# Kernel optimization log

Measured on AMD Instinct MI355X. Metric: run time of the kernel, lower is better.

The kernel has to match this reference:

```python
import jax, jax.numpy as jnp
import numpy as np

DIM = 512
NUM_HEADS = 8
HEAD_SIZE = 64
INNER = NUM_HEADS * HEAD_SIZE  # 512


def setup_inputs() -> dict:
    key = jax.random.key(0)
    k1, k2, k3, k4, k5 = jax.random.split(key, 5)
    x = jax.random.normal(k1, (2, 4096, DIM), dtype=jnp.float32)
    # Linear params stored as [in, out] for y = x @ W + b (same math as torch Linear)
    w_qkv = jax.random.normal(k2, (DIM, INNER * 3), dtype=jnp.float32) * (1.0 / np.sqrt(DIM))
    b_qkv = jax.random.normal(k3, (INNER * 3,), dtype=jnp.float32) * 0.01
    w_out = jax.random.normal(k4, (INNER, DIM), dtype=jnp.float32) * (1.0 / np.sqrt(INNER))
    b_out = jax.random.normal(k5, (DIM,), dtype=jnp.float32) * 0.01
    return {"x": x, "w_qkv": w_qkv, "b_qkv": b_qkv, "w_out": w_out, "b_out": b_out}


def reference(x, w_qkv, b_qkv, w_out, b_out):
    b, n, _ = x.shape
    qkv = x @ w_qkv + b_qkv                      # [b, n, 3*inner]
    q, k, v = jnp.split(qkv, 3, axis=-1)          # each [b, n, inner]

    def heads(t):  # 'b n (h d) -> b h n d'
        return t.reshape(b, n, NUM_HEADS, HEAD_SIZE).transpose(0, 2, 1, 3)

    q, k, v = heads(q), heads(k), heads(v)
    scores = jnp.einsum('bhnd,bhmd->bhnm', q, k) / jnp.sqrt(jnp.float32(HEAD_SIZE))
    probs = jax.nn.softmax(scores, axis=-1)       # dropout is identity in eval
    out = jnp.einsum('bhnm,bhmd->bhnd', probs, v)
    out = out.transpose(0, 2, 1, 3).reshape(b, n, INNER)  # 'b h n d -> b n (h d)'
    return out @ w_out + b_out
```

## Files before the change

kernel.cpp:

```cpp
#include <hip/hip_runtime.h>

typedef __bf16 bf16;
typedef __bf16 bf16x8 __attribute__((ext_vector_type(8)));
typedef float f32x4 __attribute__((ext_vector_type(4)));
typedef unsigned u32x4 __attribute__((ext_vector_type(4)));

#define MFMA16(a, b, c) __builtin_amdgcn_mfma_f32_16x16x32_bf16((a), (b), (c), 0, 0, 0)

static __device__ __forceinline__ bf16x8 ldg8(const bf16* p) {
  return *(const bf16x8*)p;
}
static __device__ __forceinline__ unsigned cvt_pk_bf16(float lo, float hi) {
  unsigned d;
  asm("v_cvt_pk_bf16_f32 %0, %1, %2" : "=v"(d) : "v"(lo), "v"(hi));
  return d;
}
static __device__ __forceinline__ void pl32_swap(unsigned& a, unsigned& b) {
  asm("v_permlane32_swap_b32 %0, %1" : "+v"(a), "+v"(b));
}
static __device__ __forceinline__ void pl16_swap(unsigned& a, unsigned& b) {
  asm("v_permlane16_swap_b32 %0, %1" : "+v"(a), "+v"(b));
}


__global__ __launch_bounds__(256) void cvt_pack_x(const float* __restrict__ x,
                                                  bf16* __restrict__ Xp) {
  int mt = blockIdx.x, kc = blockIdx.y;
  int r = threadIdx.x >> 1;
  int khalf = threadIdx.x & 1;
  const float* src = x + (size_t)(mt * 128 + r) * 512 + kc * 32 + khalf * 16;
  float4 v0 = *(const float4*)(src + 0);
  float4 v1 = *(const float4*)(src + 4);
  float4 v2 = *(const float4*)(src + 8);
  float4 v3 = *(const float4*)(src + 12);
  bf16* tile = Xp + ((size_t)mt * 16 + kc) * 4096;
  bf16x8 a, b;
  a[0] = (bf16)v0.x; a[1] = (bf16)v0.y; a[2] = (bf16)v0.z; a[3] = (bf16)v0.w;
  a[4] = (bf16)v1.x; a[5] = (bf16)v1.y; a[6] = (bf16)v1.z; a[7] = (bf16)v1.w;
  b[0] = (bf16)v2.x; b[1] = (bf16)v2.y; b[2] = (bf16)v2.z; b[3] = (bf16)v2.w;
  b[4] = (bf16)v3.x; b[5] = (bf16)v3.y; b[6] = (bf16)v3.z; b[7] = (bf16)v3.w;
  int kc0 = khalf * 2;
  *(bf16x8*)&tile[(kc0 + 0) * 1024 + r * 8] = a;
  *(bf16x8*)&tile[(kc0 + 1) * 1024 + r * 8] = b;
}

__global__ __launch_bounds__(256) void transpose_pack_w(const float* __restrict__ W,
                                                        bf16* __restrict__ Wp,
                                                        int N) {
  __shared__ float tile[32 * 129];
  int kc = blockIdx.x, nt = blockIdx.y;
  int row = threadIdx.x >> 3;
  int c0 = (threadIdx.x & 7) * 16;
  const float* src = W + (size_t)(kc * 32 + row) * N + nt * 128 + c0;
#pragma unroll
  for (int i = 0; i < 4; i++) {
    float4 v = *(const float4*)(src + i * 4);
    tile[row * 129 + c0 + i * 4 + 0] = v.x;
    tile[row * 129 + c0 + i * 4 + 1] = v.y;
    tile[row * 129 + c0 + i * 4 + 2] = v.z;
    tile[row * 129 + c0 + i * 4 + 3] = v.w;
  }
  __syncthreads();
  bf16* dst = Wp + ((size_t)nt * 16 + kc) * 4096;
#pragma unroll
  for (int half = 0; half < 2; half++) {
    int U = threadIdx.x + half * 256;
    int kchunk = U >> 7, n = U & 127;
    bf16x8 o;
#pragma unroll
    for (int j = 0; j < 8; j++) o[j] = (bf16)tile[(kchunk * 8 + j) * 129 + n];
    *(bf16x8*)&dst[U * 8] = o;
  }
}

__device__ __forceinline__ void gemm128_core(const bf16* __restrict__ At,
                                             const bf16* __restrict__ Bt,
                                             bf16* Ab0, bf16* Ab1, bf16* Bb0,
                                             bf16* Bb1, int tid, int wr, int wc,
                                             int l16, int quad, f32x4 acc[4][4]) {
  bf16x8 pa0 = ldg8(At + tid * 8);
  bf16x8 pa1 = ldg8(At + 2048 + tid * 8);
  bf16x8 pb0 = ldg8(Bt + tid * 8);
  bf16x8 pb1 = ldg8(Bt + 2048 + tid * 8);
#pragma unroll 2
  for (int kc = 0; kc < 16; kc++) {
    bf16* Ab = (kc & 1) ? Ab1 : Ab0;
    bf16* Bb = (kc & 1) ? Bb1 : Bb0;
    *(bf16x8*)&Ab[tid * 8] = pa0;
    *(bf16x8*)&Ab[2048 + tid * 8] = pa1;
    *(bf16x8*)&Bb[tid * 8] = pb0;
    *(bf16x8*)&Bb[2048 + tid * 8] = pb1;
    __syncthreads();
    if (kc < 15) {
      const bf16* an = At + (kc + 1) * 4096;
      const bf16* bn = Bt + (kc + 1) * 4096;
      pa0 = ldg8(an + tid * 8);
      pa1 = ldg8(an + 2048 + tid * 8);
      pb0 = ldg8(bn + tid * 8);
      pb1 = ldg8(bn + 2048 + tid * 8);
    }
    bf16x8 af[4], bf[4];
#pragma unroll
    for (int fi = 0; fi < 4; fi++)
      af[fi] = *(const bf16x8*)&Ab[(quad * 128 + wr * 64 + fi * 16 + l16) * 8];
#pragma unroll
    for (int fj = 0; fj < 4; fj++)
      bf[fj] = *(const bf16x8*)&Bb[(quad * 128 + wc * 64 + fj * 16 + l16) * 8];
    __builtin_amdgcn_s_setprio(1);
#pragma unroll
    for (int fi = 0; fi < 4; fi++)
#pragma unroll
      for (int fj = 0; fj < 4; fj++)
        acc[fi][fj] = MFMA16(af[fi], bf[fj], acc[fi][fj]);
    __builtin_amdgcn_s_setprio(0);
  }
}

__global__ __launch_bounds__(256, 3) void qkv_gemm(const bf16* __restrict__ Xp,
                                                   const bf16* __restrict__ Wp1,
                                                   const float* __restrict__ bqkv,
                                                   bf16* __restrict__ Q,
                                                   bf16* __restrict__ Kh,
                                                   bf16* __restrict__ Vt) {
  int mt = blockIdx.x, nt = blockIdx.y;
  int tid = threadIdx.x;
  int wave = tid >> 6, lane = tid & 63;
  int l16 = lane & 15, quad = lane >> 4;
  int wr = wave >> 1, wc = wave & 1;

  __shared__ __align__(16) bf16 Ab[2][4096];
  __shared__ __align__(16) bf16 Bb[2][4096];

  f32x4 acc[4][4] = {};
  gemm128_core(Xp + (size_t)mt * 16 * 4096, Wp1 + (size_t)nt * 16 * 4096,
               Ab[0], Ab[1], Bb[0], Bb[1], tid, wr, wc, l16, quad, acc);

#pragma unroll
  for (int fj = 0; fj < 4; fj++) {
    int c = nt * 128 + wc * 64 + fj * 16 + l16;
    float bias = bqkv[c];
    int which = c >> 9, inner = c & 511;
    int h = inner >> 6, d = inner & 63;
#pragma unroll
    for (int fi = 0; fi < 4; fi++) {
#pragma unroll
      for (int r = 0; r < 4; r++) {
        int m = mt * 128 + wr * 64 + fi * 16 + quad * 4 + r;
        int b = m >> 12, n = m & 4095;
        int bh = b * 8 + h;
        float v = acc[fi][fj][r] + bias;
        if (which == 0)
          Q[((size_t)bh * 4096 + n) * 64 + d] = (bf16)(v * 0.18033688f);
        else if (which == 1)
          Kh[((size_t)bh * 4096 + n) * 64 + d] = (bf16)v;
        else
          Vt[(((size_t)bh * 64 + (n >> 6)) * 64 + d) * 64 + (n & 63)] = (bf16)v;
      }
    }
  }
}

__global__ __launch_bounds__(256, 4) void flash_partial(const bf16* __restrict__ Q,
                                                        const bf16* __restrict__ K,
                                                        const bf16* __restrict__ Vt,
                                                        bf16* __restrict__ Opart,
                                                        float* __restrict__ Lpart) {
  int strip = blockIdx.x, bh = blockIdx.y, half = blockIdx.z;
  int tid = threadIdx.x;
  int wave = tid >> 6, lane = tid & 63;
  int l16 = lane & 15, quad = lane >> 4;

  const bf16* Qh = Q + (size_t)bh * 4096 * 64;
  const bf16* Kg = K + ((size_t)bh * 4096 + half * 2048) * 64;
  const bf16* Vg = Vt + (size_t)bh * 64 * 4096 + (size_t)half * 2048 * 64;

  __shared__ __align__(16) bf16 Klds[2][4096];
  __shared__ __align__(16) bf16 Vlds[2][4096];

  int qbase = strip * 128 + wave * 32;
  bf16x8 aq[2][2];
#pragma unroll
  for (int mt = 0; mt < 2; mt++) {
    const bf16* qr = Qh + (size_t)(qbase + mt * 16 + l16) * 64;
    aq[mt][0] = ldg8(qr + quad * 8);
    aq[mt][1] = ldg8(qr + 32 + quad * 8);
  }

  bf16x8 ones;
#pragma unroll
  for (int i = 0; i < 8; i++) ones[i] = (bf16)1.0f;

  f32x4 o[2][4] = {};
  f32x4 acc_l[2] = {};

  int e0 = tid * 8, e1 = (256 + tid) * 8;
  int r0 = e0 >> 6, r1 = e1 >> 6;
  int u0 = r0 * 8 + (((e0 & 63) >> 3) ^ (r0 & 7));
  int u1 = r1 * 8 + (((e1 & 63) >> 3) ^ (r1 & 7));

  bf16x8 kp0 = ldg8(Kg + e0), kp1 = ldg8(Kg + e1);
  bf16x8 vp0 = ldg8(Vg + e0), vp1 = ldg8(Vg + e1);

#pragma unroll 2
  for (int t = 0; t < 32; t++) {
    int cur = t & 1;
    bf16* kl = Klds[cur];
    bf16* vl = Vlds[cur];
    *(bf16x8*)&kl[u0 * 8] = kp0;
    *(bf16x8*)&kl[u1 * 8] = kp1;
    *(bf16x8*)&vl[u0 * 8] = vp0;
    *(bf16x8*)&vl[u1 * 8] = vp1;
    __syncthreads();

    if (t < 31) {
      const bf16* kg = Kg + (size_t)(t + 1) * 4096;
      const bf16* vg = Vg + (size_t)(t + 1) * 4096;
      kp0 = ldg8(kg + e0);
      kp1 = ldg8(kg + e1);
      vp0 = ldg8(vg + e0);
      vp1 = ldg8(vg + e1);
    }

    f32x4 s[2][2][2] = {};
    __builtin_amdgcn_s_setprio(1);
#pragma unroll
    for (int h2 = 0; h2 < 2; h2++)
#pragma unroll
      for (int c2 = 0; c2 < 2; c2++) {
        int n = h2 * 32 + c2 * 16 + l16;
        bf16x8 k0 = *(const bf16x8*)&kl[(n * 8 + (quad ^ (n & 7))) * 8];
        bf16x8 k1 = *(const bf16x8*)&kl[(n * 8 + ((4 + quad) ^ (n & 7))) * 8];
#pragma unroll
        for (int mt = 0; mt < 2; mt++) {
          s[h2][mt][c2] = MFMA16(k0, aq[mt][0], s[h2][mt][c2]);
          s[h2][mt][c2] = MFMA16(k1, aq[mt][1], s[h2][mt][c2]);
        }
      }
    __builtin_amdgcn_s_setprio(0);

    bf16x8 pa[2][2];
#pragma unroll
    for (int h2 = 0; h2 < 2; h2++)
#pragma unroll
      for (int mt = 0; mt < 2; mt++) {
        unsigned ue[2], wo[2];
#pragma unroll
        for (int c2 = 0; c2 < 2; c2++) {
          float p0 = __builtin_amdgcn_exp2f(s[h2][mt][c2][0]);
          float p1 = __builtin_amdgcn_exp2f(s[h2][mt][c2][1]);
          float p2 = __builtin_amdgcn_exp2f(s[h2][mt][c2][2]);
          float p3 = __builtin_amdgcn_exp2f(s[h2][mt][c2][3]);
          ue[c2] = cvt_pk_bf16(p0, p1);
          wo[c2] = cvt_pk_bf16(p2, p3);
        }
        pl32_swap(ue[0], ue[1]);
        pl16_swap(ue[0], ue[1]);
        pl32_swap(wo[0], wo[1]);
        pl16_swap(wo[0], wo[1]);
        u32x4 pk = {ue[0], wo[0], ue[1], wo[1]};
        pa[h2][mt] = __builtin_bit_cast(bf16x8, pk);
      }

    __builtin_amdgcn_s_setprio(1);
    acc_l[0] = MFMA16(pa[0][0], ones, acc_l[0]);
    acc_l[1] = MFMA16(pa[0][1], ones, acc_l[1]);
    acc_l[0] = MFMA16(pa[1][0], ones, acc_l[0]);
    acc_l[1] = MFMA16(pa[1][1], ones, acc_l[1]);
#pragma unroll
    for (int h2 = 0; h2 < 2; h2++)
#pragma unroll
      for (int ct = 0; ct < 4; ct++) {
        int d = ct * 16 + l16;
        bf16x8 bv = *(const bf16x8*)&vl[(d * 8 + ((h2 * 4 + quad) ^ (d & 7))) * 8];
        o[0][ct] = MFMA16(pa[h2][0], bv, o[0][ct]);
        o[1][ct] = MFMA16(pa[h2][1], bv, o[1][ct]);
      }
    __builtin_amdgcn_s_setprio(0);
  }

  size_t ub = ((size_t)half * 16 + bh) * 32 + strip;
  bf16* op = Opart + ub * 8192;
#pragma unroll
  for (int mt = 0; mt < 2; mt++) {
#pragma unroll
    for (int ct = 0; ct < 4; ct++)
#pragma unroll
      for (int r = 0; r < 4; r++)
        op[(wave * 32 + mt * 16 + quad * 4 + r) * 64 + ct * 16 + l16] =
            (bf16)o[mt][ct][r];
    if (l16 == 0) {
#pragma unroll
      for (int r = 0; r < 4; r++)
        Lpart[ub * 128 + wave * 32 + mt * 16 + quad * 4 + r] = acc_l[mt][r];
    }
  }
}

__global__ __launch_bounds__(256) void flash_combine(const bf16* __restrict__ Opart,
                                                     const float* __restrict__ Lpart,
                                                     bf16* __restrict__ Ap) {
  int mt = blockIdx.x, kc = blockIdx.y;
  int b = mt >> 5, strip = mt & 31;
  int h = kc >> 1, d0 = (kc & 1) * 32;
  int bh = b * 8 + h;
  size_t u0 = (size_t)bh * 32 + strip;
  size_t u1 = ((size_t)16 + bh) * 32 + strip;
  bf16* dst = Ap + ((size_t)mt * 16 + kc) * 4096;
#pragma unroll
  for (int hf = 0; hf < 2; hf++) {
    int U = threadIdx.x + hf * 256;
    int kchunk = U >> 7, r = U & 127;
    bf16x8 o0 = ldg8(&Opart[u0 * 8192 + r * 64 + d0 + kchunk * 8]);
    bf16x8 o1 = ldg8(&Opart[u1 * 8192 + r * 64 + d0 + kchunk * 8]);
    float ls = Lpart[u0 * 128 + r] + Lpart[u1 * 128 + r];
    float rl = 1.0f / ls;
    bf16x8 ov;
#pragma unroll
    for (int j = 0; j < 8; j++) ov[j] = (bf16)(((float)o0[j] + (float)o1[j]) * rl);
    *(bf16x8*)&dst[U * 8] = ov;
  }
}

__global__ __launch_bounds__(256, 3) void out_gemm(const bf16* __restrict__ Ap,
                                                   const bf16* __restrict__ Wp2,
                                                   const float* __restrict__ bout,
                                                   float* __restrict__ Out) {
  int mt = blockIdx.x, nt = blockIdx.y;
  int tid = threadIdx.x;
  int wave = tid >> 6, lane = tid & 63;
  int l16 = lane & 15, quad = lane >> 4;
  int wr = wave >> 1, wc = wave & 1;

  __shared__ __align__(16) bf16 Ab[2][4096];
  __shared__ __align__(16) bf16 Bb[2][4096];

  f32x4 acc[4][4] = {};
  gemm128_core(Ap + (size_t)mt * 16 * 4096, Wp2 + (size_t)nt * 16 * 4096,
               Ab[0], Ab[1], Bb[0], Bb[1], tid, wr, wc, l16, quad, acc);

#pragma unroll
  for (int fj = 0; fj < 4; fj++) {
    int c = nt * 128 + wc * 64 + fj * 16 + l16;
    float bias = bout[c];
#pragma unroll
    for (int fi = 0; fi < 4; fi++) {
#pragma unroll
      for (int r = 0; r < 4; r++) {
        int m = mt * 128 + wr * 64 + fi * 16 + quad * 4 + r;
        Out[(size_t)m * 512 + c] = acc[fi][fj][r] + bias;
      }
    }
  }
}

extern "C" void kernel_launch(void* const* d_in, const int* in_sizes, int n_in,
                              void* d_out, int out_size, void* d_ws,
                              size_t ws_size, hipStream_t stream) {
  const float* x = (const float*)d_in[0];
  const float* w_qkv = (const float*)d_in[1];
  const float* b_qkv = (const float*)d_in[2];
  const float* w_out = (const float*)d_in[3];
  const float* b_out = (const float*)d_in[4];
  float* out = (float*)d_out;

  char* ws = (char*)d_ws;
  bf16* Q = (bf16*)(ws + 0);
  bf16* K = (bf16*)(ws + 8388608);
  bf16* Vt = (bf16*)(ws + 16777216);
  bf16* Wp2 = (bf16*)(ws + 25165824);
  bf16* Opart = (bf16*)(ws + 25690112);
  float* Lpart = (float*)(ws + 42467328);
  bf16* Xp = (bf16*)(ws + 42991616);
  bf16* Wp1 = (bf16*)(ws + 51380224);
  bf16* Ap = (bf16*)(ws + 52953088);

  cvt_pack_x<<<dim3(64, 16), 256, 0, stream>>>(x, Xp);
  transpose_pack_w<<<dim3(16, 12), 256, 0, stream>>>(w_qkv, Wp1, 1536);
  transpose_pack_w<<<dim3(16, 4), 256, 0, stream>>>(w_out, Wp2, 512);
  qkv_gemm<<<dim3(64, 12), 256, 0, stream>>>(Xp, Wp1, b_qkv, Q, K, Vt);
  flash_partial<<<dim3(32, 16, 2), 256, 0, stream>>>(Q, K, Vt, Opart, Lpart);
  flash_combine<<<dim3(64, 16), 256, 0, stream>>>(Opart, Lpart, Ap);
  out_gemm<<<dim3(64, 4), 256, 0, stream>>>(Ap, Wp2, b_out, out);
}
```

Before: 206.5 us.

## Split attention keys four ways, restructure softmax loop, async LDS loads in GEMMs

Attention is now split into four key chunks instead of two, giving twice as many blocks to fill the GPU, and the combine kernel sums four partials. The per-tile score loop is restructured to finish each 32-key half before starting the next, lowering live registers. The GEMM core now copies global memory straight into LDS with global_load_lds instead of passing through registers, with the barrier moved to the end of the loop. The workspace is re-laid out with aliased buffers to fit the larger partial output, at the cost of more combine traffic.

```diff
diff --git a/kernel.cpp b/kernel.cpp
--- a/kernel.cpp
+++ b/kernel.cpp
@@ -4,6 +4,7 @@
 typedef __bf16 bf16x8 __attribute__((ext_vector_type(8)));
 typedef float f32x4 __attribute__((ext_vector_type(4)));
 typedef unsigned u32x4 __attribute__((ext_vector_type(4)));
+typedef unsigned u32;
 
 #define MFMA16(a, b, c) __builtin_amdgcn_mfma_f32_16x16x32_bf16((a), (b), (c), 0, 0, 0)
 
@@ -20,6 +21,11 @@
 }
 static __device__ __forceinline__ void pl16_swap(unsigned& a, unsigned& b) {
   asm("v_permlane16_swap_b32 %0, %1" : "+v"(a), "+v"(b));
+}
+static __device__ __forceinline__ void async_lds16(const bf16* g, bf16* l) {
+  __builtin_amdgcn_global_load_lds(
+      (const __attribute__((address_space(1))) u32*)(const void*)g,
+      (__attribute__((address_space(3))) u32*)(void*)l, 16, 0, 0);
 }
 
 
@@ -73,31 +79,33 @@
   }
 }
 
+static __device__ __forceinline__ void stage_tile(const bf16* __restrict__ g,
+                                                  bf16* l, int wave, int lane) {
+#pragma unroll
+  for (int c = 0; c < 2; c++) {
+    int chunk = wave * 2 + c;
+    async_lds16(g + chunk * 512 + lane * 8, l + chunk * 512);
+  }
+}
+
 __device__ __forceinline__ void gemm128_core(const bf16* __restrict__ At,
                                              const bf16* __restrict__ Bt,
                                              bf16* Ab0, bf16* Ab1, bf16* Bb0,
-                                             bf16* Bb1, int tid, int wr, int wc,
-                                             int l16, int quad, f32x4 acc[4][4]) {
-  bf16x8 pa0 = ldg8(At + tid * 8);
-  bf16x8 pa1 = ldg8(At + 2048 + tid * 8);
-  bf16x8 pb0 = ldg8(Bt + tid * 8);
-  bf16x8 pb1 = ldg8(Bt + 2048 + tid * 8);
+                                             bf16* Bb1, int wave, int lane,
+                                             int wr, int wc, int l16, int quad,
+                                             f32x4 acc[4][4]) {
+  stage_tile(At, Ab0, wave, lane);
+  stage_tile(Bt, Bb0, wave, lane);
+  __syncthreads();
 #pragma unroll 2
   for (int kc = 0; kc < 16; kc++) {
     bf16* Ab = (kc & 1) ? Ab1 : Ab0;
     bf16* Bb = (kc & 1) ? Bb1 : Bb0;
-    *(bf16x8*)&Ab[tid * 8] = pa0;
-    *(bf16x8*)&Ab[2048 + tid * 8] = pa1;
-    *(bf16x8*)&Bb[tid * 8] = pb0;
-    *(bf16x8*)&Bb[2048 + tid * 8] = pb1;
-    __syncthreads();
     if (kc < 15) {
-      const bf16* an = At + (kc + 1) * 4096;
-      const bf16* bn = Bt + (kc + 1) * 4096;
-      pa0 = ldg8(an + tid * 8);
-      pa1 = ldg8(an + 2048 + tid * 8);
-      pb0 = ldg8(bn + tid * 8);
-      pb1 = ldg8(bn + 2048 + tid * 8);
+      bf16* An = (kc & 1) ? Ab0 : Ab1;
+      bf16* Bn = (kc & 1) ? Bb0 : Bb1;
+      stage_tile(At + (kc + 1) * 4096, An, wave, lane);
+      stage_tile(Bt + (kc + 1) * 4096, Bn, wave, lane);
     }
     bf16x8 af[4], bf[4];
 #pragma unroll
@@ -113,6 +121,7 @@
       for (int fj = 0; fj < 4; fj++)
         acc[fi][fj] = MFMA16(af[fi], bf[fj], acc[fi][fj]);
     __builtin_amdgcn_s_setprio(0);
+    __syncthreads();
   }
 }
 
@@ -133,7 +142,7 @@
 
   f32x4 acc[4][4] = {};
   gemm128_core(Xp + (size_t)mt * 16 * 4096, Wp1 + (size_t)nt * 16 * 4096,
-               Ab[0], Ab[1], Bb[0], Bb[1], tid, wr, wc, l16, quad, acc);
+               Ab[0], Ab[1], Bb[0], Bb[1], wave, lane, wr, wc, l16, quad, acc);
 
 #pragma unroll
   for (int fj = 0; fj < 4; fj++) {
@@ -165,14 +174,14 @@
                                                         const bf16* __restrict__ Vt,
                                                         bf16* __restrict__ Opart,
                                                         float* __restrict__ Lpart) {
-  int strip = blockIdx.x, bh = blockIdx.y, half = blockIdx.z;
+  int strip = blockIdx.x, bh = blockIdx.y, qtr = blockIdx.z;
   int tid = threadIdx.x;
   int wave = tid >> 6, lane = tid & 63;
   int l16 = lane & 15, quad = lane >> 4;
 
   const bf16* Qh = Q + (size_t)bh * 4096 * 64;
-  const bf16* Kg = K + ((size_t)bh * 4096 + half * 2048) * 64;
-  const bf16* Vg = Vt + (size_t)bh * 64 * 4096 + (size_t)half * 2048 * 64;
+  const bf16* Kg = K + ((size_t)bh * 4096 + qtr * 1024) * 64;
+  const bf16* Vg = Vt + (size_t)bh * 64 * 4096 + (size_t)qtr * 1024 * 64;
 
   __shared__ __align__(16) bf16 Klds[2][4096];
   __shared__ __align__(16) bf16 Vlds[2][4096];
@@ -202,7 +211,7 @@
   bf16x8 vp0 = ldg8(Vg + e0), vp1 = ldg8(Vg + e1);
 
 #pragma unroll 2
-  for (int t = 0; t < 32; t++) {
+  for (int t = 0; t < 16; t++) {
     int cur = t & 1;
     bf16* kl = Klds[cur];
     bf16* vl = Vlds[cur];
@@ -212,7 +221,7 @@
     *(bf16x8*)&vl[u1 * 8] = vp1;
     __syncthreads();
 
-    if (t < 31) {
+    if (t < 15) {
       const bf16* kg = Kg + (size_t)(t + 1) * 4096;
       const bf16* vg = Vg + (size_t)(t + 1) * 4096;
       kp0 = ldg8(kg + e0);
@@ -221,10 +230,10 @@
       vp1 = ldg8(vg + e1);
     }
 
-    f32x4 s[2][2][2] = {};
-    __builtin_amdgcn_s_setprio(1);
-#pragma unroll
-    for (int h2 = 0; h2 < 2; h2++)
+#pragma unroll
+    for (int h2 = 0; h2 < 2; h2++) {
+      f32x4 s[2][2] = {};
+      __builtin_amdgcn_s_setprio(1);
 #pragma unroll
       for (int c2 = 0; c2 < 2; c2++) {
         int n = h2 * 32 + c2 * 16 + l16;
@@ -232,24 +241,22 @@
         bf16x8 k1 = *(const bf16x8*)&kl[(n * 8 + ((4 + quad) ^ (n & 7))) * 8];
 #pragma unroll
         for (int mt = 0; mt < 2; mt++) {
-          s[h2][mt][c2] = MFMA16(k0, aq[mt][0], s[h2][mt][c2]);
-          s[h2][mt][c2] = MFMA16(k1, aq[mt][1], s[h2][mt][c2]);
+          s[mt][c2] = MFMA16(k0, aq[mt][0], s[mt][c2]);
+          s[mt][c2] = MFMA16(k1, aq[mt][1], s[mt][c2]);
         }
       }
-    __builtin_amdgcn_s_setprio(0);
-
-    bf16x8 pa[2][2];
-#pragma unroll
-    for (int h2 = 0; h2 < 2; h2++)
+      __builtin_amdgcn_s_setprio(0);
+
+      bf16x8 pa[2];
 #pragma unroll
       for (int mt = 0; mt < 2; mt++) {
         unsigned ue[2], wo[2];
 #pragma unroll
         for (int c2 = 0; c2 < 2; c2++) {
-          float p0 = __builtin_amdgcn_exp2f(s[h2][mt][c2][0]);
-          float p1 = __builtin_amdgcn_exp2f(s[h2][mt][c2][1]);
-          float p2 = __builtin_amdgcn_exp2f(s[h2][mt][c2][2]);
-          float p3 = __builtin_amdgcn_exp2f(s[h2][mt][c2][3]);
+          float p0 = __builtin_amdgcn_exp2f(s[mt][c2][0]);
+          float p1 = __builtin_amdgcn_exp2f(s[mt][c2][1]);
+          float p2 = __builtin_amdgcn_exp2f(s[mt][c2][2]);
+          float p3 = __builtin_amdgcn_exp2f(s[mt][c2][3]);
           ue[c2] = cvt_pk_bf16(p0, p1);
           wo[c2] = cvt_pk_bf16(p2, p3);
         }
@@ -258,27 +265,24 @@
         pl32_swap(wo[0], wo[1]);
         pl16_swap(wo[0], wo[1]);
         u32x4 pk = {ue[0], wo[0], ue[1], wo[1]};
-        pa[h2][mt] = __builtin_bit_cast(bf16x8, pk);
-      }
-
-    __builtin_amdgcn_s_setprio(1);
-    acc_l[0] = MFMA16(pa[0][0], ones, acc_l[0]);
-    acc_l[1] = MFMA16(pa[0][1], ones, acc_l[1]);
-    acc_l[0] = MFMA16(pa[1][0], ones, acc_l[0]);
-    acc_l[1] = MFMA16(pa[1][1], ones, acc_l[1]);
-#pragma unroll
-    for (int h2 = 0; h2 < 2; h2++)
+        pa[mt] = __builtin_bit_cast(bf16x8, pk);
+      }
+
+      __builtin_amdgcn_s_setprio(1);
+      acc_l[0] = MFMA16(pa[0], ones, acc_l[0]);
+      acc_l[1] = MFMA16(pa[1], ones, acc_l[1]);
 #pragma unroll
       for (int ct = 0; ct < 4; ct++) {
         int d = ct * 16 + l16;
         bf16x8 bv = *(const bf16x8*)&vl[(d * 8 + ((h2 * 4 + quad) ^ (d & 7))) * 8];
-        o[0][ct] = MFMA16(pa[h2][0], bv, o[0][ct]);
-        o[1][ct] = MFMA16(pa[h2][1], bv, o[1][ct]);
-      }
-    __builtin_amdgcn_s_setprio(0);
-  }
-
-  size_t ub = ((size_t)half * 16 + bh) * 32 + strip;
+        o[0][ct] = MFMA16(pa[0], bv, o[0][ct]);
+        o[1][ct] = MFMA16(pa[1], bv, o[1][ct]);
+      }
+      __builtin_amdgcn_s_setprio(0);
+    }
+  }
+
+  size_t ub = ((size_t)qtr * 16 + bh) * 32 + strip;
   bf16* op = Opart + ub * 8192;
 #pragma unroll
   for (int mt = 0; mt < 2; mt++) {
@@ -303,21 +307,28 @@
   int b = mt >> 5, strip = mt & 31;
   int h = kc >> 1, d0 = (kc & 1) * 32;
   int bh = b * 8 + h;
-  size_t u0 = (size_t)bh * 32 + strip;
-  size_t u1 = ((size_t)16 + bh) * 32 + strip;
+  size_t u[4];
+#pragma unroll
+  for (int q = 0; q < 4; q++) u[q] = ((size_t)q * 16 + bh) * 32 + strip;
   bf16* dst = Ap + ((size_t)mt * 16 + kc) * 4096;
 #pragma unroll
   for (int hf = 0; hf < 2; hf++) {
     int U = threadIdx.x + hf * 256;
     int kchunk = U >> 7, r = U & 127;
-    bf16x8 o0 = ldg8(&Opart[u0 * 8192 + r * 64 + d0 + kchunk * 8]);
-    bf16x8 o1 = ldg8(&Opart[u1 * 8192 + r * 64 + d0 + kchunk * 8]);
-    float ls = Lpart[u0 * 128 + r] + Lpart[u1 * 128 + r];
+    float acc[8] = {};
+    float ls = 0.f;
+#pragma unroll
+    for (int q = 0; q < 4; q++) {
+      bf16x8 ov = ldg8(&Opart[u[q] * 8192 + r * 64 + d0 + kchunk * 8]);
+#pragma unroll
+      for (int j = 0; j < 8; j++) acc[j] += (float)ov[j];
+      ls += Lpart[u[q] * 128 + r];
+    }
     float rl = 1.0f / ls;
-    bf16x8 ov;
-#pragma unroll
-    for (int j = 0; j < 8; j++) ov[j] = (bf16)(((float)o0[j] + (float)o1[j]) * rl);
-    *(bf16x8*)&dst[U * 8] = ov;
+    bf16x8 o;
+#pragma unroll
+    for (int j = 0; j < 8; j++) o[j] = (bf16)(acc[j] * rl);
+    *(bf16x8*)&dst[U * 8] = o;
   }
 }
 
@@ -336,7 +347,7 @@
 
   f32x4 acc[4][4] = {};
   gemm128_core(Ap + (size_t)mt * 16 * 4096, Wp2 + (size_t)nt * 16 * 4096,
-               Ab[0], Ab[1], Bb[0], Bb[1], tid, wr, wc, l16, quad, acc);
+               Ab[0], Ab[1], Bb[0], Bb[1], wave, lane, wr, wc, l16, quad, acc);
 
 #pragma unroll
   for (int fj = 0; fj < 4; fj++) {
@@ -369,16 +380,16 @@
   bf16* Vt = (bf16*)(ws + 16777216);
   bf16* Wp2 = (bf16*)(ws + 25165824);
   bf16* Opart = (bf16*)(ws + 25690112);
-  float* Lpart = (float*)(ws + 42467328);
-  bf16* Xp = (bf16*)(ws + 42991616);
-  bf16* Wp1 = (bf16*)(ws + 51380224);
-  bf16* Ap = (bf16*)(ws + 52953088);
+  float* Lpart = (float*)(ws + 59244544);
+  bf16* Xp = (bf16*)(ws + 25690112);
+  bf16* Wp1 = (bf16*)(ws + 34078720);
+  bf16* Ap = (bf16*)(ws + 0);
 
   cvt_pack_x<<<dim3(64, 16), 256, 0, stream>>>(x, Xp);
   transpose_pack_w<<<dim3(16, 12), 256, 0, stream>>>(w_qkv, Wp1, 1536);
   transpose_pack_w<<<dim3(16, 4), 256, 0, stream>>>(w_out, Wp2, 512);
   qkv_gemm<<<dim3(64, 12), 256, 0, stream>>>(Xp, Wp1, b_qkv, Q, K, Vt);
-  flash_partial<<<dim3(32, 16, 2), 256, 0, stream>>>(Q, K, Vt, Opart, Lpart);
+  flash_partial<<<dim3(32, 16, 4), 256, 0, stream>>>(Q, K, Vt, Opart, Lpart);
   flash_combine<<<dim3(64, 16), 256, 0, stream>>>(Opart, Lpart, Ap);
   out_gemm<<<dim3(64, 4), 256, 0, stream>>>(Ap, Wp2, b_out, out);
 }
```

After: 208.2 us. No clear change (+0.8%).
